# Optimization experiments

Hardware: AMD Instinct MI355X
Metric: run time of the kernel (lower is better)

The kernel has to match this reference:

```python
import jax, jax.numpy as jnp
import numpy as np

DIM = 768
HEADS = 12
HEAD_DIM = DIM // HEADS


def setup_inputs() -> dict:
    key = jax.random.key(0)
    ks = jax.random.split(key, 6)
    B, Nq, Nkv = 2, 2048, 2048
    s = 0.02
    return {
        "query_source": jax.random.normal(ks[0], (B, Nq, DIM), jnp.float32),
        "kv_source": jax.random.normal(ks[1], (B, Nkv, DIM), jnp.float32),
        "Wq": jax.random.normal(ks[2], (DIM, DIM), jnp.float32) * s,
        "Wkv": jax.random.normal(ks[3], (DIM, 2 * DIM), jnp.float32) * s,
        "Wproj": jax.random.normal(ks[4], (DIM, DIM), jnp.float32) * s,
        "bproj": jax.random.normal(ks[5], (DIM,), jnp.float32) * s,
    }


def reference(query_source, kv_source, Wq, Wkv, Wproj, bproj):
    B, Nq, D = query_source.shape
    Nkv = kv_source.shape[1]
    scale = HEAD_DIM ** -0.5
    # projections (qkv_bias=False)
    q = (query_source @ Wq).reshape(B, Nq, HEADS, HEAD_DIM)
    kv = (kv_source @ Wkv).reshape(B, Nkv, 2, HEADS, HEAD_DIM)
    k, v = kv[:, :, 0], kv[:, :, 1]  # (B, Nkv, H, Dh)
    # scores: (B, H, Nq, Nkv)
    attn = jnp.einsum("bqhd,bkhd->bhqk", q, k) * scale
    attn = jax.nn.softmax(attn, axis=-1)
    # attn_drop = 0 (eval)
    x = jnp.einsum("bhqk,bkhd->bqhd", attn, v).reshape(B, Nq, D)
    return x @ Wproj + bproj
```

## Files before the change

kernel.cpp:

```cpp
#include <hip/hip_runtime.h>
#include <math.h>
#include <stdint.h>

typedef __bf16 bf16_t;
typedef __attribute__((ext_vector_type(8))) __bf16 bf16x8;
typedef __attribute__((ext_vector_type(4))) __bf16 bf16x4;
typedef __attribute__((ext_vector_type(4))) float f32x4;

#define DIM   768
#define HEADS 12
#define HD    64
#define NB    2
#define NQ    2048
#define NKV   2048
#define MROWS 4096
#define NQKV  2304

__device__ __forceinline__ float fast_exp2(float x)
{
#if __has_builtin(__builtin_amdgcn_exp2f)
    return __builtin_amdgcn_exp2f(x);
#else
    return exp2f(x);
#endif
}

__device__ __forceinline__ uint32_t pack_bf16x2(float a, float b)
{
    const uint32_t lo = __builtin_bit_cast(uint32_t, a) + 0x8000u;
    const uint32_t hi = __builtin_bit_cast(uint32_t, b) + 0x8000u;
#if __has_builtin(__builtin_amdgcn_perm)
    return __builtin_amdgcn_perm(hi, lo, 0x07060302u);
#else
    return (lo >> 16) | (hi & 0xffff0000u);
#endif
}

__device__ __forceinline__ void async_copy16(const bf16_t* g, bf16_t* l)
{
    typedef const __attribute__((address_space(1))) uint32_t* gp_t;
    typedef __attribute__((address_space(3))) uint32_t* lp_t;
    __builtin_amdgcn_global_load_lds((gp_t)(const void*)g, (lp_t)(void*)l, 16, 0, 0);
}

__global__ void prep_kernel(const float* __restrict__ qs, bf16_t* __restrict__ qs_bf,
                            const float* __restrict__ kvs, bf16_t* __restrict__ kvs_bf,
                            const float* __restrict__ Wq, const float* __restrict__ Wkv,
                            const float* __restrict__ Wproj, bf16_t* __restrict__ Wt,
                            float escale)
{
    __shared__ float tile[32][33];
    const int z = blockIdx.z;
    if (z < 2) {
        const float* in  = z ? kvs : qs;
        bf16_t*      out = z ? kvs_bf : qs_bf;
        const int i = (blockIdx.x * 256 + threadIdx.x) * 8;
        bf16x8 v;
#pragma unroll
        for (int j = 0; j < 8; j++) v[j] = (bf16_t)in[i + j];
        *(bf16x8*)(out + i) = v;
        return;
    }
    const int N   = (z == 3) ? 2 * DIM : DIM;
    const int nb  = N / 32;
    const int idx = blockIdx.x;
    if (idx >= nb * (DIM / 32)) return;
    const float* W = (z == 2) ? Wq : (z == 3) ? Wkv : Wproj;
    bf16_t* T = Wt + ((z == 2) ? (size_t)0 : (z == 3) ? (size_t)DIM * DIM
                                                      : (size_t)NQKV * DIM);
    const float scl = (z == 2) ? escale : 1.0f;
    const int n0 = (idx % nb) * 32, k0 = (idx / nb) * 32;
    const int tx = threadIdx.x & 31, ty = threadIdx.x >> 5;
#pragma unroll
    for (int i = 0; i < 4; i++)
        tile[ty + i * 8][tx] = W[(size_t)(k0 + ty + i * 8) * N + n0 + tx];
    __syncthreads();
#pragma unroll
    for (int i = 0; i < 4; i++)
        T[(size_t)(n0 + ty + i * 8) * DIM + k0 + tx] = (bf16_t)(tile[tx][ty + i * 8] * scl);
}

template<int MODE, int TN>
__global__ __launch_bounds__(256)
void gemm_bk64(const bf16_t* __restrict__ Aq, const bf16_t* __restrict__ Akv,
               const bf16_t* __restrict__ Bt,
               bf16_t* __restrict__ Qb, bf16_t* __restrict__ Kb, bf16_t* __restrict__ Vtb,
               float* __restrict__ ofp, const float* __restrict__ bias)
{
    constexpr int K  = DIM;
    constexpr int NT = TN / 32;
    constexpr int ABLK = 128 * 64;
    constexpr int BBLK = TN * 64;
    constexpr int STEP = ABLK + BBLK;
    constexpr int TRELEMS = (MODE == 0) ? 128 * 136 : 0;
    constexpr int SELEMS = (2 * STEP > TRELEMS) ? 2 * STEP : TRELEMS;
    __shared__ __align__(16) bf16_t smem[SELEMS];

    const int tid  = threadIdx.x;
    const int wave = tid >> 6, lane = tid & 63;
    const int quad = lane >> 4, l16 = lane & 15, l7 = l16 & 7;
    const int bm = blockIdx.x * 128, bn = blockIdx.y * TN;
    const int wm = (wave >> 1) * 64, wn = (wave & 1) * (TN / 2);

    const bf16_t* A = (MODE == 0) ? (bn < DIM ? Aq : Akv) : Aq;

    const int srow = tid >> 3;
    const int scol = ((tid & 7) ^ (srow & 7)) * 8;
    const bf16_t* Ag[4];
    const bf16_t* Bg[NT];
#pragma unroll
    for (int i = 0; i < 4; i++)
        Ag[i] = A + (size_t)(bm + i * 32 + srow) * K + scol;
#pragma unroll
    for (int i = 0; i < NT; i++)
        Bg[i] = Bt + (size_t)(bn + i * 32 + srow) * K + scol;

    f32x4 acc[4][NT] = {};

    {
        bf16_t* AsL = smem + tid * 8;
        bf16_t* BsL = smem + ABLK + tid * 8;
#pragma unroll
        for (int i = 0; i < 4; i++) async_copy16(Ag[i], AsL + i * 2048);
#pragma unroll
        for (int i = 0; i < NT; i++) async_copy16(Bg[i], BsL + i * 2048);
    }
    __syncthreads();

    for (int t = 0; t < K / 64; t++) {
        bf16_t* Ac = smem + (t & 1) * STEP;
        bf16_t* Bc = Ac + ABLK;

        if (t + 1 < K / 64) {
            bf16_t* AsL = smem + ((t + 1) & 1) * STEP + tid * 8;
            bf16_t* BsL = AsL + ABLK;
            const int k1 = (t + 1) * 64;
#pragma unroll
            for (int i = 0; i < 4; i++) async_copy16(Ag[i] + k1, AsL + i * 2048);
#pragma unroll
            for (int i = 0; i < NT; i++) async_copy16(Bg[i] + k1, BsL + i * 2048);
        }

#pragma unroll
        for (int ks = 0; ks < 2; ks++) {
            const int pc = ((ks * 4 + quad) ^ l7) * 8;
            bf16x8 af[4], bfr[NT];
#pragma unroll
            for (int mt = 0; mt < 4; mt++)
                af[mt] = *(const bf16x8*)(&Ac[(wm + mt * 16 + l16) * 64 + pc]);
#pragma unroll
            for (int nt = 0; nt < NT; nt++)
                bfr[nt] = *(const bf16x8*)(&Bc[(wn + nt * 16 + l16) * 64 + pc]);
#pragma unroll
            for (int mt = 0; mt < 4; mt++)
#pragma unroll
                for (int nt = 0; nt < NT; nt++)
                    acc[mt][nt] = __builtin_amdgcn_mfma_f32_16x16x32_bf16(
                        af[mt], bfr[nt], acc[mt][nt], 0, 0, 0);
        }

        __syncthreads();
    }

    if (MODE == 1) {
#pragma unroll
        for (int mt = 0; mt < 4; mt++)
#pragma unroll
            for (int nt = 0; nt < NT; nt++)
#pragma unroll
                for (int r = 0; r < 4; r++) {
                    const int gm = bm + wm + mt * 16 + quad * 4 + r;
                    const int gn = bn + wn + nt * 16 + l16;
                    ofp[(size_t)gm * DIM + gn] = acc[mt][nt][r] + bias[gn];
                }
    } else if (bn < DIM) {
#pragma unroll
        for (int mt = 0; mt < 4; mt++)
#pragma unroll
            for (int nt = 0; nt < NT; nt++)
#pragma unroll
                for (int r = 0; r < 4; r++) {
                    const int gm = bm + wm + mt * 16 + quad * 4 + r;
                    const int gn = bn + wn + nt * 16 + l16;
                    Qb[(size_t)gm * DIM + gn] = (bf16_t)acc[mt][nt][r];
                }
    } else if (bn < 2 * DIM) {
#pragma unroll
        for (int mt = 0; mt < 4; mt++)
#pragma unroll
            for (int nt = 0; nt < NT; nt++)
#pragma unroll
                for (int r = 0; r < 4; r++) {
                    const int gm = bm + wm + mt * 16 + quad * 4 + r;
                    const int gn = bn + wn + nt * 16 + l16 - DIM;
                    Kb[(size_t)gm * DIM + gn] = (bf16_t)acc[mt][nt][r];
                }
    } else {
        bf16_t* tr = smem;
#pragma unroll
        for (int mt = 0; mt < 4; mt++)
#pragma unroll
            for (int nt = 0; nt < NT; nt++) {
                bf16x4 tv;
#pragma unroll
                for (int r = 0; r < 4; r++) tv[r] = (bf16_t)acc[mt][nt][r];
                *(bf16x4*)(&tr[(wn + nt * 16 + l16) * 136 + wm + mt * 16 + quad * 4]) = tv;
            }
        __syncthreads();
        const int b = bm >> 11, kv0 = bm & 2047;
        const int n2base = bn - 2 * DIM;
        const int cg = tid & 15, cc = cg >> 2, cq = cg & 3;
#pragma unroll
        for (int i = 0; i < TN / 16; i++) {
            const int row = i * 16 + (tid >> 4);
            const int n2 = n2base + row, h = n2 >> 6, d = n2 & 63;
            const bf16x4 lo4 = *(const bf16x4*)(&tr[row * 136 + cc * 32 + cq * 4]);
            const bf16x4 hi4 = *(const bf16x4*)(&tr[row * 136 + cc * 32 + 16 + cq * 4]);
            bf16x8 vv;
#pragma unroll
            for (int j = 0; j < 4; j++) { vv[j] = lo4[j]; vv[4 + j] = hi4[j]; }
            *(bf16x8*)(Vtb + ((size_t)(b * HEADS + h) * HD + d) * NKV + kv0 + cg * 8) = vv;
        }
    }
}

__global__ __launch_bounds__(256, 4)
void attn_kernel(const bf16_t* __restrict__ Qb, const bf16_t* __restrict__ Kb,
                 const bf16_t* __restrict__ Vt, bf16_t* __restrict__ Xb)
{
    __shared__ __align__(16) bf16_t kvbuf[2][8192];

    const int tid  = threadIdx.x;
    const int wave = tid >> 6, lane = tid & 63;
    const int quad = lane >> 4, l16 = lane & 15;
    const int l7   = l16 & 7;

    const int id   = blockIdx.x + (NB * HEADS) * blockIdx.y;
    const int xcd  = id & 7, slot = id >> 3;
    const int bh   = xcd + 8 * (slot >> 5);
    const int b = bh / HEADS, h = bh % HEADS;
    const int q0 = (slot & 31) * 64;

    const bf16_t* Qp = Qb + (size_t)b * NQ * DIM + h * HD;
    const bf16_t* Kp = Kb + (size_t)b * NKV * DIM + h * HD;
    const bf16_t* Vp = Vt + (size_t)(b * HEADS + h) * HD * NKV;

    const int sr = tid >> 3, sp = tid & 7;
    const bf16_t* KgA = Kp + (size_t)sr * DIM + ((sp ^ (sr & 7)) * 8);
    const bf16_t* VgA = Vp + (size_t)sr * NKV + ((sp ^ (sr & 7)) * 8);

    {
        bf16_t* kb = kvbuf[0] + tid * 8;
#pragma unroll
        for (int i = 0; i < 2; i++)
            async_copy16(KgA + (size_t)(i * 32) * DIM, kb + i * 2048);
#pragma unroll
        for (int i = 0; i < 2; i++)
            async_copy16(VgA + (size_t)(i * 32) * NKV, kb + 4096 + i * 2048);
    }

    bf16x8 qf[2];
#pragma unroll
    for (int ks = 0; ks < 2; ks++)
        qf[ks] = *(const bf16x8*)(Qp + (size_t)(q0 + wave * 16 + l16) * DIM
                                  + ks * 32 + quad * 8);

    f32x4 o[4] = {};
    float li = 0.0f;

    __syncthreads();

    for (int t = 0; t < NKV / 64; t++) {
        const bf16_t* kv = kvbuf[t & 1];

        if (t + 1 < NKV / 64) {
            bf16_t* kb = kvbuf[(t + 1) & 1] + tid * 8;
            const int kv1 = (t + 1) * 64;
#pragma unroll
            for (int i = 0; i < 2; i++)
                async_copy16(KgA + (size_t)(kv1 + i * 32) * DIM, kb + i * 2048);
#pragma unroll
            for (int i = 0; i < 2; i++)
                async_copy16(VgA + (size_t)(i * 32) * NKV + kv1, kb + 4096 + i * 2048);
        }

        f32x4 s[4] = {};
        __builtin_amdgcn_s_setprio(1);
#pragma unroll
        for (int kt = 0; kt < 4; kt++)
#pragma unroll
            for (int ks = 0; ks < 2; ks++) {
                const bf16x8 kf = *(const bf16x8*)(&kv[
                    (kt * 16 + l16) * 64 + (((ks * 4 + quad) ^ l7) * 8)]);
                s[kt] = __builtin_amdgcn_mfma_f32_16x16x32_bf16(kf, qf[ks], s[kt], 0, 0, 0);
            }
        __builtin_amdgcn_s_setprio(0);

        float p[16];
#pragma unroll
        for (int kt = 0; kt < 4; kt++)
#pragma unroll
            for (int r = 0; r < 4; r++) p[kt * 4 + r] = fast_exp2(s[kt][r]);
        float rs = 0.0f;
#pragma unroll
        for (int j = 0; j < 16; j++) rs += p[j];
        li += rs;
        bf16x8 pb[2];
#pragma unroll
        for (int kc = 0; kc < 2; kc++) {
            union { uint32_t u[4]; bf16x8 v; } pu;
#pragma unroll
            for (int i = 0; i < 4; i++)
                pu.u[i] = pack_bf16x2(p[kc * 8 + 2 * i], p[kc * 8 + 2 * i + 1]);
            pb[kc] = pu.v;
        }

        __builtin_amdgcn_s_setprio(1);
#pragma unroll
        for (int dt = 0; dt < 4; dt++)
#pragma unroll
            for (int kc = 0; kc < 2; kc++) {
                const bf16x8 vf = *(const bf16x8*)(&kv[
                    4096 + (dt * 16 + l16) * 64 + (((kc * 4 + quad) ^ l7) * 8)]);
                o[dt] = __builtin_amdgcn_mfma_f32_16x16x32_bf16(vf, pb[kc], o[dt], 0, 0, 0);
            }
        __builtin_amdgcn_s_setprio(0);

        __syncthreads();
    }

    li += __shfl_xor(li, 16);
    li += __shfl_xor(li, 32);
    const float inv = 1.0f / li;

    bf16_t* Ob16 = &kvbuf[0][0];
#pragma unroll
    for (int dt = 0; dt < 4; dt++) {
        bf16x4 ov;
#pragma unroll
        for (int r = 0; r < 4; r++) ov[r] = (bf16_t)(o[dt][r] * inv);
        *(bf16x4*)(&Ob16[(wave * 16 + l16) * 72 + dt * 16 + quad * 4]) = ov;
    }
    __syncthreads();
    {
        const int row = tid >> 2, ch = (tid & 3) * 16;
        bf16_t* dst = Xb + (size_t)(b * NQ + q0 + row) * DIM + h * HD + ch;
        *(bf16x8*)(dst)     = *(const bf16x8*)(&Ob16[row * 72 + ch]);
        *(bf16x8*)(dst + 8) = *(const bf16x8*)(&Ob16[row * 72 + ch + 8]);
    }
}

extern "C" void kernel_launch(void* const* d_in, const int* in_sizes, int n_in,
                              void* d_out, int out_size, void* d_ws, size_t ws_size,
                              hipStream_t stream)
{
    const float* qs    = (const float*)d_in[0];
    const float* kvs   = (const float*)d_in[1];
    const float* Wq    = (const float*)d_in[2];
    const float* Wkv   = (const float*)d_in[3];
    const float* Wproj = (const float*)d_in[4];
    const float* bproj = (const float*)d_in[5];
    float* out = (float*)d_out;

    bf16_t* w = (bf16_t*)d_ws;
    bf16_t* qs_bf  = w;  w += (size_t)MROWS * DIM;
    bf16_t* kvs_bf = w;  w += (size_t)MROWS * DIM;
    bf16_t* Wt     = w;  w += (size_t)NQKV * DIM;
    bf16_t* Wprojt = w;  w += (size_t)DIM * DIM;
    bf16_t* Qb     = w;  w += (size_t)MROWS * DIM;
    bf16_t* Kb     = w;  w += (size_t)MROWS * DIM;
    bf16_t* Vtb    = w;  w += (size_t)MROWS * DIM;
    bf16_t* Xb     = qs_bf;

    const float escale = 0.125f * 1.44269504088896341f;
    prep_kernel<<<dim3(MROWS * DIM / 2048, 1, 5), 256, 0, stream>>>(
        qs, qs_bf, kvs, kvs_bf, Wq, Wkv, Wproj, Wt, escale);

    gemm_bk64<0, 96><<<dim3(MROWS / 128, NQKV / 96), 256, 0, stream>>>(
        qs_bf, kvs_bf, Wt, Qb, Kb, Vtb, nullptr, nullptr);
    attn_kernel<<<dim3(NB * HEADS, NQ / 64), 256, 0, stream>>>(Qb, Kb, Vtb, Xb);
    gemm_bk64<1, 32><<<dim3(MROWS / 128, DIM / 32), 256, 0, stream>>>(
        Xb, nullptr, Wprojt, nullptr, nullptr, nullptr, out, bproj);
}
```

Baseline: 152.3 us.

## Split KV tiles across wave pairs in attention with 512-thread blocks

The attention kernel now uses 512 threads per block. Pairs of waves split each 64-wide KV tile so each wave handles 32 keys, and the partial outputs and row sums are merged through shared memory at the end. The double-buffered async prefetch is replaced by a single buffer that is loaded and then synchronized each iteration. This raises the number of waves per query tile and lowers per-wave register pressure, but the memory load is no longer overlapped with compute and a cross-wave reduction is added.

```diff
diff --git a/kernel.cpp b/kernel.cpp
--- a/kernel.cpp
+++ b/kernel.cpp
@@ -22,17 +22,6 @@
     return __builtin_amdgcn_exp2f(x);
 #else
     return exp2f(x);
-#endif
-}
-
-__device__ __forceinline__ uint32_t pack_bf16x2(float a, float b)
-{
-    const uint32_t lo = __builtin_bit_cast(uint32_t, a) + 0x8000u;
-    const uint32_t hi = __builtin_bit_cast(uint32_t, b) + 0x8000u;
-#if __has_builtin(__builtin_amdgcn_perm)
-    return __builtin_amdgcn_perm(hi, lo, 0x07060302u);
-#else
-    return (lo >> 16) | (hi & 0xffff0000u);
 #endif
 }
 
@@ -224,18 +213,20 @@
     }
 }
 
-__global__ __launch_bounds__(256, 4)
+__global__ __launch_bounds__(512, 6)
 void attn_kernel(const bf16_t* __restrict__ Qb, const bf16_t* __restrict__ Kb,
                  const bf16_t* __restrict__ Vt, bf16_t* __restrict__ Xb)
 {
-    __shared__ __align__(16) bf16_t kvbuf[2][8192];
+    __shared__ __align__(16) bf16_t kvbuf[8960];
+    __shared__ float libuf[4][16];
 
     const int tid  = threadIdx.x;
     const int wave = tid >> 6, lane = tid & 63;
     const int quad = lane >> 4, l16 = lane & 15;
     const int l7   = l16 & 7;
-
-    const int id   = blockIdx.x + (NB * HEADS) * blockIdx.y;
+    const int kvh = wave & 1, qh = wave >> 1;
+
+    const int id   = blockIdx.x;
     const int xcd  = id & 7, slot = id >> 3;
     const int bh   = xcd + 8 * (slot >> 5);
     const int b = bh / HEADS, h = bh % HEADS;
@@ -249,104 +240,92 @@
     const bf16_t* KgA = Kp + (size_t)sr * DIM + ((sp ^ (sr & 7)) * 8);
     const bf16_t* VgA = Vp + (size_t)sr * NKV + ((sp ^ (sr & 7)) * 8);
 
-    {
-        bf16_t* kb = kvbuf[0] + tid * 8;
-#pragma unroll
-        for (int i = 0; i < 2; i++)
-            async_copy16(KgA + (size_t)(i * 32) * DIM, kb + i * 2048);
-#pragma unroll
-        for (int i = 0; i < 2; i++)
-            async_copy16(VgA + (size_t)(i * 32) * NKV, kb + 4096 + i * 2048);
-    }
-
     bf16x8 qf[2];
 #pragma unroll
     for (int ks = 0; ks < 2; ks++)
-        qf[ks] = *(const bf16x8*)(Qp + (size_t)(q0 + wave * 16 + l16) * DIM
+        qf[ks] = *(const bf16x8*)(Qp + (size_t)(q0 + qh * 16 + l16) * DIM
                                   + ks * 32 + quad * 8);
 
     f32x4 o[4] = {};
     float li = 0.0f;
 
-    __syncthreads();
-
     for (int t = 0; t < NKV / 64; t++) {
-        const bf16_t* kv = kvbuf[t & 1];
-
-        if (t + 1 < NKV / 64) {
-            bf16_t* kb = kvbuf[(t + 1) & 1] + tid * 8;
-            const int kv1 = (t + 1) * 64;
-#pragma unroll
-            for (int i = 0; i < 2; i++)
-                async_copy16(KgA + (size_t)(kv1 + i * 32) * DIM, kb + i * 2048);
-#pragma unroll
-            for (int i = 0; i < 2; i++)
-                async_copy16(VgA + (size_t)(i * 32) * NKV + kv1, kb + 4096 + i * 2048);
-        }
-
-        f32x4 s[4] = {};
+        const int kv0 = t * 64;
+        async_copy16(KgA + (size_t)kv0 * DIM, kvbuf + tid * 8);
+        async_copy16(VgA + kv0, kvbuf + 4096 + tid * 8);
+        __syncthreads();
+
+        f32x4 s[2] = {};
         __builtin_amdgcn_s_setprio(1);
 #pragma unroll
-        for (int kt = 0; kt < 4; kt++)
+        for (int kt = 0; kt < 2; kt++)
 #pragma unroll
             for (int ks = 0; ks < 2; ks++) {
-                const bf16x8 kf = *(const bf16x8*)(&kv[
-                    (kt * 16 + l16) * 64 + (((ks * 4 + quad) ^ l7) * 8)]);
+                const bf16x8 kf = *(const bf16x8*)(&kvbuf[
+                    (kvh * 32 + kt * 16 + l16) * 64 + (((ks * 4 + quad) ^ l7) * 8)]);
                 s[kt] = __builtin_amdgcn_mfma_f32_16x16x32_bf16(kf, qf[ks], s[kt], 0, 0, 0);
             }
         __builtin_amdgcn_s_setprio(0);
 
-        float p[16];
-#pragma unroll
-        for (int kt = 0; kt < 4; kt++)
+        float p[8];
+#pragma unroll
+        for (int kt = 0; kt < 2; kt++)
 #pragma unroll
             for (int r = 0; r < 4; r++) p[kt * 4 + r] = fast_exp2(s[kt][r]);
         float rs = 0.0f;
 #pragma unroll
-        for (int j = 0; j < 16; j++) rs += p[j];
+        for (int j = 0; j < 8; j++) rs += p[j];
         li += rs;
-        bf16x8 pb[2];
-#pragma unroll
-        for (int kc = 0; kc < 2; kc++) {
-            union { uint32_t u[4]; bf16x8 v; } pu;
-#pragma unroll
-            for (int i = 0; i < 4; i++)
-                pu.u[i] = pack_bf16x2(p[kc * 8 + 2 * i], p[kc * 8 + 2 * i + 1]);
-            pb[kc] = pu.v;
-        }
+        bf16x8 pb;
+#pragma unroll
+        for (int j = 0; j < 8; j++) pb[j] = (bf16_t)p[j];
 
         __builtin_amdgcn_s_setprio(1);
 #pragma unroll
-        for (int dt = 0; dt < 4; dt++)
-#pragma unroll
-            for (int kc = 0; kc < 2; kc++) {
-                const bf16x8 vf = *(const bf16x8*)(&kv[
-                    4096 + (dt * 16 + l16) * 64 + (((kc * 4 + quad) ^ l7) * 8)]);
-                o[dt] = __builtin_amdgcn_mfma_f32_16x16x32_bf16(vf, pb[kc], o[dt], 0, 0, 0);
-            }
+        for (int dt = 0; dt < 4; dt++) {
+            const bf16x8 vf = *(const bf16x8*)(&kvbuf[
+                4096 + (dt * 16 + l16) * 64 + (((kvh * 4 + quad) ^ l7) * 8)]);
+            o[dt] = __builtin_amdgcn_mfma_f32_16x16x32_bf16(vf, pb, o[dt], 0, 0, 0);
+        }
         __builtin_amdgcn_s_setprio(0);
-
         __syncthreads();
     }
 
     li += __shfl_xor(li, 16);
     li += __shfl_xor(li, 32);
-    const float inv = 1.0f / li;
-
-    bf16_t* Ob16 = &kvbuf[0][0];
-#pragma unroll
-    for (int dt = 0; dt < 4; dt++) {
-        bf16x4 ov;
-#pragma unroll
-        for (int r = 0; r < 4; r++) ov[r] = (bf16_t)(o[dt][r] * inv);
-        *(bf16x4*)(&Ob16[(wave * 16 + l16) * 72 + dt * 16 + quad * 4]) = ov;
-    }
-    __syncthreads();
+    if (kvh == 1 && quad == 0) libuf[qh][l16] = li;
+
+    float*  R    = (float*)&kvbuf[0];
+    bf16_t* Ob16 = kvbuf + 4224;
+#pragma unroll
+    for (int ph = 0; ph < 2; ph++) {
+        if (kvh == 1 && (qh >> 1) == ph) {
+#pragma unroll
+            for (int dt = 0; dt < 4; dt++)
+#pragma unroll
+                for (int r = 0; r < 4; r++)
+                    R[(dt * 16 + quad * 4 + r) * 33 + (qh & 1) * 16 + l16] = o[dt][r];
+        }
+        __syncthreads();
+        if (kvh == 0 && (qh >> 1) == ph) {
+            const float inv = 1.0f / (li + libuf[qh][l16]);
+#pragma unroll
+            for (int dt = 0; dt < 4; dt++) {
+                bf16x4 ov;
+#pragma unroll
+                for (int r = 0; r < 4; r++)
+                    ov[r] = (bf16_t)((o[dt][r]
+                                      + R[(dt * 16 + quad * 4 + r) * 33 + (qh & 1) * 16 + l16])
+                                     * inv);
+                *(bf16x4*)(&Ob16[(qh * 16 + l16) * 72 + dt * 16 + quad * 4]) = ov;
+            }
+        }
+        __syncthreads();
+    }
     {
-        const int row = tid >> 2, ch = (tid & 3) * 16;
+        const int row = tid >> 3, ch = (tid & 7) * 8;
         bf16_t* dst = Xb + (size_t)(b * NQ + q0 + row) * DIM + h * HD + ch;
-        *(bf16x8*)(dst)     = *(const bf16x8*)(&Ob16[row * 72 + ch]);
-        *(bf16x8*)(dst + 8) = *(const bf16x8*)(&Ob16[row * 72 + ch + 8]);
+        *(bf16x8*)(dst) = *(const bf16x8*)(&Ob16[row * 72 + ch]);
     }
 }
 
@@ -378,7 +357,7 @@
 
     gemm_bk64<0, 96><<<dim3(MROWS / 128, NQKV / 96), 256, 0, stream>>>(
         qs_bf, kvs_bf, Wt, Qb, Kb, Vtb, nullptr, nullptr);
-    attn_kernel<<<dim3(NB * HEADS, NQ / 64), 256, 0, stream>>>(Qb, Kb, Vtb, Xb);
+    attn_kernel<<<dim3(768), 512, 0, stream>>>(Qb, Kb, Vtb, Xb);
     gemm_bk64<1, 32><<<dim3(MROWS / 128, DIM / 32), 256, 0, stream>>>(
         Xb, nullptr, Wprojt, nullptr, nullptr, nullptr, out, bproj);
 }
```

Result: no change. 152.5 us (+0.1%).
